# Kernel optimization log

Hardware: AMD Instinct MI355X
Metric: run time of the kernel (lower is better)

Reference implementation:

```python
import jax, jax.numpy as jnp
import numpy as np

H = 16
LN_EPS = 1e-5


def setup_inputs() -> dict:
    key = jax.random.key(0)
    ks = jax.random.split(key, 8)
    B, N, D = 2, 2048, 1024
    s = D ** -0.5
    return {
        "q_s": jax.random.normal(ks[0], (B, N, D), jnp.float32),
        "pos_emb": jax.random.normal(ks[1], (B, N, D), jnp.float32),
        "Wq": jax.random.normal(ks[2], (D, D), jnp.float32) * s,
        "Wk": jax.random.normal(ks[3], (D, D), jnp.float32) * s,
        "Wv": jax.random.normal(ks[4], (D, D), jnp.float32) * s,
        "Wo": jax.random.normal(ks[5], (D, D), jnp.float32) * s,
        "bo": jnp.zeros((D,), jnp.float32),
        "ln_g": jnp.ones((D,), jnp.float32),
        "ln_b": jnp.zeros((D,), jnp.float32),
    }


def _split_heads(t):
    b, n, d = t.shape
    return t.reshape(b, n, H, d // H).transpose(0, 2, 1, 3)  # b h n d


def reference(q_s, pos_emb, Wq, Wk, Wv, Wo, bo, ln_g, ln_b):
    # self-attention: k_s = v_s = q_s
    q = _split_heads(q_s @ Wq)
    k = _split_heads(q_s @ Wk)
    v = _split_heads(q_s @ Wv)
    p = _split_heads(pos_emb)
    scale = q.shape[-1] ** -0.5
    # content-content + content-position attention logits: [b,h,i,j]
    att = (jnp.einsum('bhid,bhjd->bhij', q, k) + jnp.einsum('bhid,bhjd->bhij', q, p)) * scale
    att = jax.nn.softmax(att, axis=-1)
    o = jnp.einsum('bhij,bhjd->bhid', att, v)
    b, h, n, d = o.shape
    o = o.transpose(0, 2, 1, 3).reshape(b, n, h * d)
    o = o @ Wo + bo  # out_layer (dropout rate 0 -> identity)
    x = o + q_s  # residual
    mu = jnp.mean(x, axis=-1, keepdims=True)
    var = jnp.var(x, axis=-1, keepdims=True)
    return (x - mu) * jax.lax.rsqrt(var + LN_EPS) * ln_g + ln_b
```

## Files before the change

### kernel.cpp

```cpp
#include <hip/hip_runtime.h>
#include <hip/hip_bf16.h>
#include <stdint.h>

typedef unsigned short u16;
typedef unsigned int u32;
typedef short s16x8 __attribute__((ext_vector_type(8)));
typedef short s16x4 __attribute__((ext_vector_type(4)));
typedef float f32x4 __attribute__((ext_vector_type(4)));

#define MFMA(a, b, c) __builtin_amdgcn_mfma_f32_16x16x32_bf16((a), (b), (c), 0, 0, 0)

__device__ __forceinline__ u16 f2bf_rte(float f) {
  __hip_bfloat16 h = __float2bfloat16(f);
  u16 u;
  __builtin_memcpy(&u, &h, 2);
  return u;
}

__device__ __forceinline__ void gload16(const u16* g, u16* l) {
  __builtin_amdgcn_global_load_lds((const __attribute__((address_space(1))) u32*)g,
                                   (__attribute__((address_space(3))) u32*)l, 16, 0, 0);
}

__global__ __launch_bounds__(256) void k_cvt(const float* __restrict__ in,
                                             u16* __restrict__ out, int n8) {
  int i = blockIdx.x * 256 + threadIdx.x;
  if (i >= n8) return;
  const f32x4* p = (const f32x4*)(in + (size_t)i * 8);
  f32x4 a = p[0], b = p[1];
  s16x8 o;
  for (int k = 0; k < 4; ++k) o[k] = (short)f2bf_rte(a[k]);
  for (int k = 0; k < 4; ++k) o[4 + k] = (short)f2bf_rte(b[k]);
  *(s16x8*)(out + (size_t)i * 8) = o;
}

__global__ __launch_bounds__(256) void k_transpose_w(const float* __restrict__ W0,
                                                     const float* __restrict__ W1,
                                                     const float* __restrict__ W2,
                                                     const float* __restrict__ W3,
                                                     u16* __restrict__ out) {
  const int z = blockIdx.z;
  const float* in = (z == 0) ? W0 : (z == 1) ? W1 : (z == 2) ? W2 : W3;
  u16* o = out + (size_t)z * 1024 * 1024;
  __shared__ u16 tile[64][65];
  const int t = threadIdx.x, tx = t & 63, ty = t >> 6;
  const int r0 = blockIdx.y * 64, c0 = blockIdx.x * 64;
  for (int rr = 0; rr < 16; ++rr) {
    int row = rr * 4 + ty;
    tile[row][tx] = f2bf_rte(in[(size_t)(r0 + row) * 1024 + c0 + tx]);
  }
  __syncthreads();
  for (int rr = 0; rr < 16; ++rr) {
    int row = rr * 4 + ty;
    o[(size_t)(c0 + row) * 1024 + r0 + tx] = tile[tx][row];
  }
}

__global__ __launch_bounds__(256) void k_transpose_v(const u16* __restrict__ V,
                                                     u16* __restrict__ Vt) {
  __shared__ u16 tile[64][65];
  const int t = threadIdx.x, tx = t & 63, ty = t >> 6;
  const int j0 = blockIdx.x * 64;
  const int bh = blockIdx.y;
  const u16* src = V + (size_t)bh * 2048 * 64;
  u16* dst = Vt + (size_t)bh * 64 * 2048;
  for (int rr = 0; rr < 16; ++rr) {
    int row = rr * 4 + ty;
    tile[row][tx] = src[(size_t)(j0 + row) * 64 + tx];
  }
  __syncthreads();
  for (int rr = 0; rr < 16; ++rr) {
    int d = rr * 4 + ty;
    dst[(size_t)d * 2048 + j0 + tx] = tile[tx][d];
  }
}

__global__ __launch_bounds__(256) void k_qkv_gemm(const u16* __restrict__ X,
                                                  const u16* __restrict__ WT,
                                                  const float* __restrict__ pos,
                                                  u16* __restrict__ Qh,
                                                  u16* __restrict__ Kh,
                                                  u16* __restrict__ Vh) {
  __shared__ u16 As[2][4096];
  __shared__ u16 Bs[2][4096];
  const int t = threadIdx.x;
  const int lane = t & 63, wid = t >> 6;
  const int wr = wid >> 1, wc = wid & 1;
  const int g = lane >> 4, lr = lane & 15;
  const int lin = blockIdx.y * 24 + blockIdx.x;
  const int swz = (lin & 7) * 96 + (lin >> 3);
  const int m0 = (swz / 24) * 128, n0 = (swz % 24) * 128;

  const int srcRow = t >> 2;
  const int srcKsw = ((t & 3) * 8) ^ (((t >> 3) & 3) << 3);
  const u16* aSrc = &X[(size_t)(m0 + srcRow) * 1024 + srcKsw];
  const u16* bSrc = &WT[(size_t)(n0 + srcRow) * 1024 + srcKsw];

  const int csw = (g * 8) ^ (((lr >> 1) & 3) << 3);

  f32x4 acc[4][4] = {};

#define QKV_STAGE(buf, k0)                                   \
  {                                                          \
    gload16(aSrc + (k0), &As[buf][wid * 512]);               \
    gload16(aSrc + 65536 + (k0), &As[buf][wid * 512 + 2048]);\
    gload16(bSrc + (k0), &Bs[buf][wid * 512]);               \
    gload16(bSrc + 65536 + (k0), &Bs[buf][wid * 512 + 2048]);\
  }

  QKV_STAGE(0, 0);
  int cur = 0;
  for (int k0 = 0; k0 < 1024; k0 += 32) {
    __syncthreads();
    if (k0 < 992) QKV_STAGE(cur ^ 1, k0 + 32);
    s16x8 a[4], b[4];
#pragma unroll
    for (int mi = 0; mi < 4; ++mi)
      a[mi] = *(const s16x8*)&As[cur][(wr * 64 + mi * 16 + lr) * 32 + csw];
#pragma unroll
    for (int nj = 0; nj < 4; ++nj)
      b[nj] = *(const s16x8*)&Bs[cur][(wc * 64 + nj * 16 + lr) * 32 + csw];
#pragma unroll
    for (int mi = 0; mi < 4; ++mi)
#pragma unroll
      for (int nj = 0; nj < 4; ++nj)
        acc[mi][nj] = MFMA(a[mi], b[nj], acc[mi][nj]);
    cur ^= 1;
  }
#undef QKV_STAGE

  const float QSCALE = 0.125f * 1.44269504f;
  for (int mi = 0; mi < 4; ++mi) {
    for (int nj = 0; nj < 4; ++nj) {
      const int n_g = n0 + wc * 64 + nj * 16 + lr;
      const int buf = n_g >> 10;
      const int col = n_g & 1023;
      const int h = col >> 6, d = col & 63;
      u16* dst = (buf == 0) ? Qh : ((buf == 1) ? Kh : Vh);
      for (int r = 0; r < 4; ++r) {
        const int row = m0 + wr * 64 + mi * 16 + g * 4 + r;
        const int b = row >> 11, n = row & 2047;
        float v = acc[mi][nj][r];
        if (buf == 1) v += pos[(size_t)row * 1024 + col];
        if (buf == 0) v *= QSCALE;
        dst[(size_t)((b * 16 + h) * 2048 + n) * 64 + d] = f2bf_rte(v);
      }
    }
  }
}

__global__ __launch_bounds__(256, 2) void k_attn(const u16* __restrict__ Qh,
                                                 const u16* __restrict__ Kh,
                                                 const u16* __restrict__ Vt,
                                                 u16* __restrict__ Oh) {
  const int t = threadIdx.x, lane = t & 63, wid = t >> 6;
  const int g = lane >> 4, lr = lane & 15;
  const int hid = blockIdx.x;
  const int lid = (hid & 7) * 64 + (hid >> 3);
  const int bh = lid >> 4, itile = lid & 15;
  const int i0 = itile * 128 + wid * 16;

  __shared__ char Ks[2][8192];
  __shared__ char Vs[2][8192];
  __shared__ char Ps[4][2][2048];

  char* Pw0 = Ps[wid][0];
  char* Pw1 = Ps[wid][1];

  const u16* Qp = Qh + (size_t)bh * 2048 * 64;
  const u16* Kp = Kh + (size_t)bh * 2048 * 64;
  const u16* Vp = Vt + (size_t)bh * 64 * 2048;

  s16x8 aq0[2], aq1[2];
  aq0[0] = *(const s16x8*)&Qp[(size_t)(i0 + lr) * 64 + g * 8];
  aq0[1] = *(const s16x8*)&Qp[(size_t)(i0 + lr) * 64 + 32 + g * 8];
  aq1[0] = *(const s16x8*)&Qp[(size_t)(i0 + 64 + lr) * 64 + g * 8];
  aq1[1] = *(const s16x8*)&Qp[(size_t)(i0 + 64 + lr) * 64 + 32 + g * 8];

  f32x4 oa0[4] = {}, oa1[4] = {};
  float m0_[4], m1_[4], l0_[4], l1_[4];
  for (int r = 0; r < 4; ++r) {
    m0_[r] = -1e30f; m1_[r] = -1e30f; l0_[r] = 0.f; l1_[r] = 0.f;
  }

  const int srow = t >> 3;
  const int sch = (t & 7) * 16;
  const int swz = (srow & 7) << 4;
  const int sb0 = (srow * 128 + sch) ^ swz;
  const int sb1 = ((srow + 32) * 128 + sch) ^ swz;
  const u16* kB0 = &Kp[(size_t)srow * 64 + (sch >> 1)];
  const u16* kB1 = &Kp[(size_t)(srow + 32) * 64 + (sch >> 1)];
  const u16* vB0 = &Vp[(size_t)srow * 2048 + (sch >> 1)];
  const u16* vB1 = &Vp[(size_t)(srow + 32) * 2048 + (sch >> 1)];

  s16x8 kr0 = *(const s16x8*)kB0;
  s16x8 kr1 = *(const s16x8*)kB1;
  s16x8 vr0 = *(const s16x8*)vB0;
  s16x8 vr1 = *(const s16x8*)vB1;
  *(s16x8*)(Ks[0] + sb0) = kr0;
  *(s16x8*)(Ks[0] + sb1) = kr1;
  *(s16x8*)(Vs[0] + sb0) = vr0;
  *(s16x8*)(Vs[0] + sb1) = vr1;
  __syncthreads();

  for (int tt = 0; tt < 32; ++tt) {
    const int cur = tt & 1;
    if (tt < 31) {
      const size_t j1 = (size_t)(tt + 1) * 64;
      kr0 = *(const s16x8*)(kB0 + j1 * 64);
      kr1 = *(const s16x8*)(kB1 + j1 * 64);
      vr0 = *(const s16x8*)(vB0 + j1);
      vr1 = *(const s16x8*)(vB1 + j1);
    }
    const char* Kc = Ks[cur];
    const char* Vc = Vs[cur];

    f32x4 s0[4] = {}, s1[4] = {};
    __builtin_amdgcn_s_setprio(1);
#pragma unroll
    for (int jf = 0; jf < 4; ++jf) {
      const int row = jf * 16 + lr;
      const int bw = (row & 7) << 4;
      s16x8 bk0 = *(const s16x8*)(Kc + ((row * 128 + g * 16) ^ bw));
      s16x8 bk1 = *(const s16x8*)(Kc + ((row * 128 + 64 + g * 16) ^ bw));
      s0[jf] = MFMA(aq0[0], bk0, s0[jf]);
      s0[jf] = MFMA(aq0[1], bk1, s0[jf]);
      s1[jf] = MFMA(aq1[0], bk0, s1[jf]);
      s1[jf] = MFMA(aq1[1], bk1, s1[jf]);
    }
    __builtin_amdgcn_s_setprio(0);

    {
      float tl[4];
      for (int r = 0; r < 4; ++r)
        tl[r] = fmaxf(fmaxf(s0[0][r], s0[1][r]), fmaxf(s0[2][r], s0[3][r]));
      int ok = (tl[0] <= m0_[0] + 8.f) & (tl[1] <= m0_[1] + 8.f) &
               (tl[2] <= m0_[2] + 8.f) & (tl[3] <= m0_[3] + 8.f);
      if (!__all(ok)) {
        for (int r = 0; r < 4; ++r) {
          float tm = tl[r];
          for (int m = 1; m < 16; m <<= 1) tm = fmaxf(tm, __shfl_xor(tm, m, 64));
          float mnew = fmaxf(m0_[r], tm);
          float alpha = __builtin_amdgcn_exp2f(m0_[r] - mnew);
          l0_[r] *= alpha;
          m0_[r] = mnew;
          for (int df = 0; df < 4; ++df) oa0[df][r] *= alpha;
        }
      }
#pragma unroll
      for (int jf = 0; jf < 4; ++jf)
        for (int r = 0; r < 4; ++r) {
          float p = __builtin_amdgcn_exp2f(s0[jf][r] - m0_[r]);
          s0[jf][r] = p;
          l0_[r] += p;
        }
    }
    {
      float tl[4];
      for (int r = 0; r < 4; ++r)
        tl[r] = fmaxf(fmaxf(s1[0][r], s1[1][r]), fmaxf(s1[2][r], s1[3][r]));
      int ok = (tl[0] <= m1_[0] + 8.f) & (tl[1] <= m1_[1] + 8.f) &
               (tl[2] <= m1_[2] + 8.f) & (tl[3] <= m1_[3] + 8.f);
      if (!__all(ok)) {
        for (int r = 0; r < 4; ++r) {
          float tm = tl[r];
          for (int m = 1; m < 16; m <<= 1) tm = fmaxf(tm, __shfl_xor(tm, m, 64));
          float mnew = fmaxf(m1_[r], tm);
          float alpha = __builtin_amdgcn_exp2f(m1_[r] - mnew);
          l1_[r] *= alpha;
          m1_[r] = mnew;
          for (int df = 0; df < 4; ++df) oa1[df][r] *= alpha;
        }
      }
#pragma unroll
      for (int jf = 0; jf < 4; ++jf)
        for (int r = 0; r < 4; ++r) {
          float p = __builtin_amdgcn_exp2f(s1[jf][r] - m1_[r]);
          s1[jf][r] = p;
          l1_[r] += p;
        }
    }

#pragma unroll
    for (int jf = 0; jf < 4; ++jf)
      for (int r = 0; r < 4; ++r) {
        const int row = g * 4 + r;
        const int off = (row * 128 + (jf * 16 + lr) * 2) ^ ((row & 7) << 4);
        *(u16*)(Pw0 + off) = f2bf_rte(s0[jf][r]);
        *(u16*)(Pw1 + off) = f2bf_rte(s1[jf][r]);
      }

    s16x8 pa0[2], pa1[2];
    {
      const int bw = (lr & 7) << 4;
      pa0[0] = *(const s16x8*)(Pw0 + ((lr * 128 + g * 16) ^ bw));
      pa0[1] = *(const s16x8*)(Pw0 + ((lr * 128 + 64 + g * 16) ^ bw));
      pa1[0] = *(const s16x8*)(Pw1 + ((lr * 128 + g * 16) ^ bw));
      pa1[1] = *(const s16x8*)(Pw1 + ((lr * 128 + 64 + g * 16) ^ bw));
    }

    __builtin_amdgcn_s_setprio(1);
#pragma unroll
    for (int df = 0; df < 4; ++df) {
      const int row = df * 16 + lr;
      const int bw = (row & 7) << 4;
      s16x8 bv0 = *(const s16x8*)(Vc + ((row * 128 + g * 16) ^ bw));
      s16x8 bv1 = *(const s16x8*)(Vc + ((row * 128 + 64 + g * 16) ^ bw));
      oa0[df] = MFMA(pa0[0], bv0, oa0[df]);
      oa0[df] = MFMA(pa0[1], bv1, oa0[df]);
      oa1[df] = MFMA(pa1[0], bv0, oa1[df]);
      oa1[df] = MFMA(pa1[1], bv1, oa1[df]);
    }
    __builtin_amdgcn_s_setprio(0);

    if (tt < 31) {
      char* Kn = Ks[cur ^ 1];
      char* Vn = Vs[cur ^ 1];
      *(s16x8*)(Kn + sb0) = kr0;
      *(s16x8*)(Kn + sb1) = kr1;
      *(s16x8*)(Vn + sb0) = vr0;
      *(s16x8*)(Vn + sb1) = vr1;
    }
    __syncthreads();
  }

  for (int r = 0; r < 4; ++r) {
    float ps = l0_[r];
    for (int m = 1; m < 16; m <<= 1) ps += __shfl_xor(ps, m, 64);
    l0_[r] = ps;
    ps = l1_[r];
    for (int m = 1; m < 16; m <<= 1) ps += __shfl_xor(ps, m, 64);
    l1_[r] = ps;
  }

  u16* Op = Oh + (size_t)bh * 2048 * 64;
#pragma unroll
  for (int df = 0; df < 4; ++df)
    for (int r = 0; r < 4; ++r) {
      const int row0 = i0 + g * 4 + r;
      Op[(size_t)row0 * 64 + df * 16 + lr] = f2bf_rte(oa0[df][r] / l0_[r]);
      Op[(size_t)(row0 + 64) * 64 + df * 16 + lr] = f2bf_rte(oa1[df][r] / l1_[r]);
    }
}

__global__ __launch_bounds__(256) void k_out_gemm(const u16* __restrict__ Oh,
                                                  const u16* __restrict__ WTo,
                                                  const float* __restrict__ bo,
                                                  const float* __restrict__ qs,
                                                  float* __restrict__ X) {
  __shared__ u16 As[2][4096];
  __shared__ u16 Bs[2][4096];
  const int t = threadIdx.x;
  const int lane = t & 63, wid = t >> 6;
  const int wr = wid >> 1, wc = wid & 1;
  const int g = lane >> 4, lr = lane & 15;
  const int lin = blockIdx.y * 8 + blockIdx.x;
  const int swz = (lin & 7) * 32 + (lin >> 3);
  const int m0 = (swz / 8) * 128, n0 = (swz % 8) * 128;

  const int srcRow = t >> 2;
  const int srcKsw = ((t & 3) * 8) ^ (((t >> 3) & 3) << 3);
  const int rg = m0 + srcRow, bb0 = rg >> 11, nn0 = rg & 2047;
  const int rg2 = rg + 64, bb2 = rg2 >> 11, nn2 = rg2 & 2047;
  const u16* bSrc = &WTo[(size_t)(n0 + srcRow) * 1024 + srcKsw];
  const int csw = (g * 8) ^ (((lr >> 1) & 3) << 3);

  f32x4 acc[4][4] = {};

#define OUT_STAGE(buf, k0)                                                        \
  {                                                                               \
    const int h_ = (k0) >> 6, d_ = ((k0) & 63) + srcKsw;                          \
    gload16(&Oh[((size_t)(bb0 * 16 + h_) * 2048 + nn0) * 64 + d_],                \
            &As[buf][wid * 512]);                                                 \
    gload16(&Oh[((size_t)(bb2 * 16 + h_) * 2048 + nn2) * 64 + d_],                \
            &As[buf][wid * 512 + 2048]);                                          \
    gload16(bSrc + (k0), &Bs[buf][wid * 512]);                                    \
    gload16(bSrc + 65536 + (k0), &Bs[buf][wid * 512 + 2048]);                     \
  }

  OUT_STAGE(0, 0);
  int cur = 0;
  for (int k0 = 0; k0 < 1024; k0 += 32) {
    __syncthreads();
    if (k0 < 992) OUT_STAGE(cur ^ 1, k0 + 32);
    s16x8 a[4], b[4];
#pragma unroll
    for (int mi = 0; mi < 4; ++mi)
      a[mi] = *(const s16x8*)&As[cur][(wr * 64 + mi * 16 + lr) * 32 + csw];
#pragma unroll
    for (int nj = 0; nj < 4; ++nj)
      b[nj] = *(const s16x8*)&Bs[cur][(wc * 64 + nj * 16 + lr) * 32 + csw];
#pragma unroll
    for (int mi = 0; mi < 4; ++mi)
#pragma unroll
      for (int nj = 0; nj < 4; ++nj)
        acc[mi][nj] = MFMA(a[mi], b[nj], acc[mi][nj]);
    cur ^= 1;
  }
#undef OUT_STAGE

  for (int mi = 0; mi < 4; ++mi) {
    for (int nj = 0; nj < 4; ++nj) {
      const int col = n0 + wc * 64 + nj * 16 + lr;
      for (int r = 0; r < 4; ++r) {
        const int row = m0 + wr * 64 + mi * 16 + g * 4 + r;
        float v = acc[mi][nj][r] + bo[col] + qs[(size_t)row * 1024 + col];
        X[(size_t)row * 1024 + col] = v;
      }
    }
  }
}

__global__ __launch_bounds__(256) void k_ln(const float* __restrict__ X,
                                            const float* __restrict__ gg,
                                            const float* __restrict__ bb,
                                            float* __restrict__ out) {
  const int row = blockIdx.x, t = threadIdx.x;
  const int wid = t >> 6, lane = t & 63;
  const float* xr = X + (size_t)row * 1024;
  f32x4 x = *(const f32x4*)&xr[t * 4];
  float s1 = x[0] + x[1] + x[2] + x[3];
  float s2 = x[0] * x[0] + x[1] * x[1] + x[2] * x[2] + x[3] * x[3];
  for (int off = 32; off > 0; off >>= 1) {
    s1 += __shfl_down(s1, off, 64);
    s2 += __shfl_down(s2, off, 64);
  }
  __shared__ float red[2][4];
  if (lane == 0) { red[0][wid] = s1; red[1][wid] = s2; }
  __syncthreads();
  s1 = red[0][0] + red[0][1] + red[0][2] + red[0][3];
  s2 = red[1][0] + red[1][1] + red[1][2] + red[1][3];
  const float mu = s1 * (1.f / 1024.f);
  const float var = s2 * (1.f / 1024.f) - mu * mu;
  const float rstd = rsqrtf(var + 1e-5f);
  f32x4 gv = *(const f32x4*)&gg[t * 4];
  f32x4 bv = *(const f32x4*)&bb[t * 4];
  f32x4 ov;
  for (int i = 0; i < 4; ++i) ov[i] = (x[i] - mu) * rstd * gv[i] + bv[i];
  *(f32x4*)&out[(size_t)row * 1024 + t * 4] = ov;
}

extern "C" void kernel_launch(void* const* d_in, const int* in_sizes, int n_in,
                              void* d_out, int out_size, void* d_ws, size_t ws_size,
                              hipStream_t stream) {
  (void)in_sizes; (void)n_in; (void)out_size; (void)ws_size;
  const float* q_s = (const float*)d_in[0];
  const float* pos = (const float*)d_in[1];
  const float* Wq = (const float*)d_in[2];
  const float* Wk = (const float*)d_in[3];
  const float* Wv = (const float*)d_in[4];
  const float* Wo = (const float*)d_in[5];
  const float* bo = (const float*)d_in[6];
  const float* lng = (const float*)d_in[7];
  const float* lnb = (const float*)d_in[8];
  float* out = (float*)d_out;

  u16* ws = (u16*)d_ws;
  const size_t MB1 = 1024 * 1024;
  u16* WT  = ws;
  u16* Xbf = ws + 4 * MB1;
  u16* Qh  = Xbf + 4 * MB1;
  u16* Kh  = Qh + 4 * MB1;
  u16* Vh  = Kh + 4 * MB1;
  u16* Vt  = Vh + 4 * MB1;
  u16* Oh  = Vt + 4 * MB1;
  float* Xb = (float*)Qh;

  dim3 blk(256);
  k_cvt<<<dim3(2048), blk, 0, stream>>>(q_s, Xbf, 4 * MB1 / 8);
  k_transpose_w<<<dim3(16, 16, 4), blk, 0, stream>>>(Wq, Wk, Wv, Wo, WT);
  k_qkv_gemm<<<dim3(24, 32), blk, 0, stream>>>(Xbf, WT, pos, Qh, Kh, Vh);
  k_transpose_v<<<dim3(32, 32), blk, 0, stream>>>(Vh, Vt);
  k_attn<<<dim3(512), blk, 0, stream>>>(Qh, Kh, Vt, Oh);
  k_out_gemm<<<dim3(8, 32), blk, 0, stream>>>(Oh, WT + 3 * MB1, bo, q_s, Xb);
  k_ln<<<4096, blk, 0, stream>>>(Xb, lng, lnb, out);
}
```

Baseline: 158.1 us.

## Transpose QK^T MFMA and pass P to PV via shuffles instead of LDS

Result: no change. 155.4 us (-1.7%).

```diff
diff --git a/kernel.cpp b/kernel.cpp
--- a/kernel.cpp
+++ b/kernel.cpp
@@ -162,10 +162,6 @@
 
   __shared__ char Ks[2][8192];
   __shared__ char Vs[2][8192];
-  __shared__ char Ps[4][2][2048];
-
-  char* Pw0 = Ps[wid][0];
-  char* Pw1 = Ps[wid][1];
 
   const u16* Qp = Qh + (size_t)bh * 2048 * 64;
   const u16* Kp = Kh + (size_t)bh * 2048 * 64;
@@ -178,10 +174,7 @@
   aq1[1] = *(const s16x8*)&Qp[(size_t)(i0 + 64 + lr) * 64 + 32 + g * 8];
 
   f32x4 oa0[4] = {}, oa1[4] = {};
-  float m0_[4], m1_[4], l0_[4], l1_[4];
-  for (int r = 0; r < 4; ++r) {
-    m0_[r] = -1e30f; m1_[r] = -1e30f; l0_[r] = 0.f; l1_[r] = 0.f;
-  }
+  float m0s = -1e30f, m1s = -1e30f, l0s = 0.f, l1s = 0.f;
 
   const int srow = t >> 3;
   const int sch = (t & 7) * 16;
@@ -203,6 +196,9 @@
   *(s16x8*)(Vs[0] + sb1) = vr1;
   __syncthreads();
 
+  const int src0 = ((g & 1) * 2) * 16 + lr;
+  const int src1 = src0 + 16;
+
   for (int tt = 0; tt < 32; ++tt) {
     const int cur = tt & 1;
     if (tt < 31) {
@@ -223,80 +219,96 @@
       const int bw = (row & 7) << 4;
       s16x8 bk0 = *(const s16x8*)(Kc + ((row * 128 + g * 16) ^ bw));
       s16x8 bk1 = *(const s16x8*)(Kc + ((row * 128 + 64 + g * 16) ^ bw));
-      s0[jf] = MFMA(aq0[0], bk0, s0[jf]);
-      s0[jf] = MFMA(aq0[1], bk1, s0[jf]);
-      s1[jf] = MFMA(aq1[0], bk0, s1[jf]);
-      s1[jf] = MFMA(aq1[1], bk1, s1[jf]);
+      s0[jf] = MFMA(bk0, aq0[0], s0[jf]);
+      s0[jf] = MFMA(bk1, aq0[1], s0[jf]);
+      s1[jf] = MFMA(bk0, aq1[0], s1[jf]);
+      s1[jf] = MFMA(bk1, aq1[1], s1[jf]);
     }
     __builtin_amdgcn_s_setprio(0);
 
-    {
-      float tl[4];
-      for (int r = 0; r < 4; ++r)
-        tl[r] = fmaxf(fmaxf(s0[0][r], s0[1][r]), fmaxf(s0[2][r], s0[3][r]));
-      int ok = (tl[0] <= m0_[0] + 8.f) & (tl[1] <= m0_[1] + 8.f) &
-               (tl[2] <= m0_[2] + 8.f) & (tl[3] <= m0_[3] + 8.f);
-      if (!__all(ok)) {
-        for (int r = 0; r < 4; ++r) {
-          float tm = tl[r];
-          for (int m = 1; m < 16; m <<= 1) tm = fmaxf(tm, __shfl_xor(tm, m, 64));
-          float mnew = fmaxf(m0_[r], tm);
-          float alpha = __builtin_amdgcn_exp2f(m0_[r] - mnew);
-          l0_[r] *= alpha;
-          m0_[r] = mnew;
-          for (int df = 0; df < 4; ++df) oa0[df][r] *= alpha;
+    float tl0 = s0[0][0], tl1 = s1[0][0];
+#pragma unroll
+    for (int jf = 0; jf < 4; ++jf)
+#pragma unroll
+      for (int r = 0; r < 4; ++r) {
+        if (jf | r) {
+          tl0 = fmaxf(tl0, s0[jf][r]);
+          tl1 = fmaxf(tl1, s1[jf][r]);
         }
       }
-#pragma unroll
-      for (int jf = 0; jf < 4; ++jf)
-        for (int r = 0; r < 4; ++r) {
-          float p = __builtin_amdgcn_exp2f(s0[jf][r] - m0_[r]);
-          s0[jf][r] = p;
-          l0_[r] += p;
-        }
-    }
-    {
-      float tl[4];
-      for (int r = 0; r < 4; ++r)
-        tl[r] = fmaxf(fmaxf(s1[0][r], s1[1][r]), fmaxf(s1[2][r], s1[3][r]));
-      int ok = (tl[0] <= m1_[0] + 8.f) & (tl[1] <= m1_[1] + 8.f) &
-               (tl[2] <= m1_[2] + 8.f) & (tl[3] <= m1_[3] + 8.f);
-      if (!__all(ok)) {
-        for (int r = 0; r < 4; ++r) {
-          float tm = tl[r];
-          for (int m = 1; m < 16; m <<= 1) tm = fmaxf(tm, __shfl_xor(tm, m, 64));
-          float mnew = fmaxf(m1_[r], tm);
-          float alpha = __builtin_amdgcn_exp2f(m1_[r] - mnew);
-          l1_[r] *= alpha;
-          m1_[r] = mnew;
-          for (int df = 0; df < 4; ++df) oa1[df][r] *= alpha;
+    int ok = (tl0 <= m0s + 8.f) & (tl1 <= m1s + 8.f);
+    if (!__all(ok)) {
+      float tm0 = fmaxf(tl0, __shfl_xor(tl0, 16, 64));
+      tm0 = fmaxf(tm0, __shfl_xor(tm0, 32, 64));
+      float tm1 = fmaxf(tl1, __shfl_xor(tl1, 16, 64));
+      tm1 = fmaxf(tm1, __shfl_xor(tm1, 32, 64));
+      float mn0 = fmaxf(m0s, tm0), mn1 = fmaxf(m1s, tm1);
+      float al0 = __builtin_amdgcn_exp2f(m0s - mn0);
+      float al1 = __builtin_amdgcn_exp2f(m1s - mn1);
+      l0s *= al0; m0s = mn0;
+      l1s *= al1; m1s = mn1;
+#pragma unroll
+      for (int r = 0; r < 4; ++r) {
+        float ab0 = __shfl(al0, g * 4 + r, 64);
+        float ab1 = __shfl(al1, g * 4 + r, 64);
+#pragma unroll
+        for (int df = 0; df < 4; ++df) {
+          oa0[df][r] *= ab0;
+          oa1[df][r] *= ab1;
         }
       }
-#pragma unroll
-      for (int jf = 0; jf < 4; ++jf)
-        for (int r = 0; r < 4; ++r) {
-          float p = __builtin_amdgcn_exp2f(s1[jf][r] - m1_[r]);
-          s1[jf][r] = p;
-          l1_[r] += p;
-        }
     }
 
 #pragma unroll
     for (int jf = 0; jf < 4; ++jf)
+#pragma unroll
       for (int r = 0; r < 4; ++r) {
-        const int row = g * 4 + r;
-        const int off = (row * 128 + (jf * 16 + lr) * 2) ^ ((row & 7) << 4);
-        *(u16*)(Pw0 + off) = f2bf_rte(s0[jf][r]);
-        *(u16*)(Pw1 + off) = f2bf_rte(s1[jf][r]);
+        float p0 = __builtin_amdgcn_exp2f(s0[jf][r] - m0s);
+        float p1 = __builtin_amdgcn_exp2f(s1[jf][r] - m1s);
+        s0[jf][r] = p0; l0s += p0;
+        s1[jf][r] = p1; l1s += p1;
       }
 
+    u32 pk0[4][2], pk1[4][2];
+#pragma unroll
+    for (int jf = 0; jf < 4; ++jf) {
+      asm("v_cvt_pk_bf16_f32 %0, %1, %2" : "=v"(pk0[jf][0]) : "v"(s0[jf][0]), "v"(s0[jf][1]));
+      asm("v_cvt_pk_bf16_f32 %0, %1, %2" : "=v"(pk0[jf][1]) : "v"(s0[jf][2]), "v"(s0[jf][3]));
+      asm("v_cvt_pk_bf16_f32 %0, %1, %2" : "=v"(pk1[jf][0]) : "v"(s1[jf][0]), "v"(s1[jf][1]));
+      asm("v_cvt_pk_bf16_f32 %0, %1, %2" : "=v"(pk1[jf][1]) : "v"(s1[jf][2]), "v"(s1[jf][3]));
+    }
+
     s16x8 pa0[2], pa1[2];
-    {
-      const int bw = (lr & 7) << 4;
-      pa0[0] = *(const s16x8*)(Pw0 + ((lr * 128 + g * 16) ^ bw));
-      pa0[1] = *(const s16x8*)(Pw0 + ((lr * 128 + 64 + g * 16) ^ bw));
-      pa1[0] = *(const s16x8*)(Pw1 + ((lr * 128 + g * 16) ^ bw));
-      pa1[1] = *(const s16x8*)(Pw1 + ((lr * 128 + 64 + g * 16) ^ bw));
+#pragma unroll
+    for (int c = 0; c < 2; ++c) {
+      u32 a0 = (u32)__shfl((int)pk0[2 * c][0], src0, 64);
+      u32 a1 = (u32)__shfl((int)pk0[2 * c][1], src0, 64);
+      u32 a2 = (u32)__shfl((int)pk0[2 * c][0], src1, 64);
+      u32 a3 = (u32)__shfl((int)pk0[2 * c][1], src1, 64);
+      u32 b0 = (u32)__shfl((int)pk0[2 * c + 1][0], src0, 64);
+      u32 b1 = (u32)__shfl((int)pk0[2 * c + 1][1], src0, 64);
+      u32 b2 = (u32)__shfl((int)pk0[2 * c + 1][0], src1, 64);
+      u32 b3 = (u32)__shfl((int)pk0[2 * c + 1][1], src1, 64);
+      u32 w[4];
+      w[0] = (g & 2) ? b0 : a0;
+      w[1] = (g & 2) ? b1 : a1;
+      w[2] = (g & 2) ? b2 : a2;
+      w[3] = (g & 2) ? b3 : a3;
+      __builtin_memcpy(&pa0[c], w, 16);
+      u32 c0 = (u32)__shfl((int)pk1[2 * c][0], src0, 64);
+      u32 c1 = (u32)__shfl((int)pk1[2 * c][1], src0, 64);
+      u32 c2 = (u32)__shfl((int)pk1[2 * c][0], src1, 64);
+      u32 c3 = (u32)__shfl((int)pk1[2 * c][1], src1, 64);
+      u32 d0 = (u32)__shfl((int)pk1[2 * c + 1][0], src0, 64);
+      u32 d1 = (u32)__shfl((int)pk1[2 * c + 1][1], src0, 64);
+      u32 d2 = (u32)__shfl((int)pk1[2 * c + 1][0], src1, 64);
+      u32 d3 = (u32)__shfl((int)pk1[2 * c + 1][1], src1, 64);
+      u32 x[4];
+      x[0] = (g & 2) ? d0 : c0;
+      x[1] = (g & 2) ? d1 : c1;
+      x[2] = (g & 2) ? d2 : c2;
+      x[3] = (g & 2) ? d3 : c3;
+      __builtin_memcpy(&pa1[c], x, 16);
     }
 
     __builtin_amdgcn_s_setprio(1);
@@ -324,22 +336,26 @@
     __syncthreads();
   }
 
+  l0s += __shfl_xor(l0s, 16, 64);
+  l0s += __shfl_xor(l0s, 32, 64);
+  l1s += __shfl_xor(l1s, 16, 64);
+  l1s += __shfl_xor(l1s, 32, 64);
+
+  float lb0[4], lb1[4];
+#pragma unroll
   for (int r = 0; r < 4; ++r) {
-    float ps = l0_[r];
-    for (int m = 1; m < 16; m <<= 1) ps += __shfl_xor(ps, m, 64);
-    l0_[r] = ps;
-    ps = l1_[r];
-    for (int m = 1; m < 16; m <<= 1) ps += __shfl_xor(ps, m, 64);
-    l1_[r] = ps;
+    lb0[r] = __shfl(l0s, g * 4 + r, 64);
+    lb1[r] = __shfl(l1s, g * 4 + r, 64);
   }
 
   u16* Op = Oh + (size_t)bh * 2048 * 64;
 #pragma unroll
   for (int df = 0; df < 4; ++df)
+#pragma unroll
     for (int r = 0; r < 4; ++r) {
       const int row0 = i0 + g * 4 + r;
-      Op[(size_t)row0 * 64 + df * 16 + lr] = f2bf_rte(oa0[df][r] / l0_[r]);
-      Op[(size_t)(row0 + 64) * 64 + df * 16 + lr] = f2bf_rte(oa1[df][r] / l1_[r]);
+      Op[(size_t)row0 * 64 + df * 16 + lr] = f2bf_rte(oa0[df][r] / lb0[r]);
+      Op[(size_t)(row0 + 64) * 64 + df * 16 + lr] = f2bf_rte(oa1[df][r] / lb1[r]);
     }
 }
 
```
